# Optimization experiments

Hardware: AMD Instinct MI355X
Metric: run time of the kernel (lower is better)

The kernel has to match this reference:

```python
import jax, jax.numpy as jnp
import numpy as np
import math

SEQ = 2048
N_EMBD = 2048
N_HEAD = 16
DIM = N_EMBD // N_HEAD  # 128


def setup_inputs() -> dict:
    key = jax.random.key(0)
    k1, k2, k3, k4, k5 = jax.random.split(key, 5)
    s = 1.0 / math.sqrt(N_EMBD)
    return {
        "hidden_states": jax.random.normal(k1, (SEQ, N_EMBD), dtype=jnp.float32),
        "Wqkv": jax.random.normal(k2, (N_HEAD, N_EMBD, 3 * DIM), dtype=jnp.float32) * s,
        "bqkv": jax.random.normal(k3, (N_HEAD, 3 * DIM), dtype=jnp.float32) * 0.02,
        "Wout": jax.random.normal(k4, (N_EMBD, N_EMBD), dtype=jnp.float32) * s,
        "bout": jax.random.normal(k5, (N_EMBD,), dtype=jnp.float32) * 0.02,
    }


def reference(hidden_states, Wqkv, bqkv, Wout, bout):
    # per-head qkv projection: [h, s, 3*dim]
    qkv = jnp.einsum("se,hed->hsd", hidden_states, Wqkv) + bqkv[:, None, :]
    q, k, v = qkv[..., :DIM], qkv[..., DIM:2 * DIM], qkv[..., 2 * DIM:]
    # NOTE: original divides by sqrt(n_embd), not sqrt(head_dim)
    scale = 1.0 / math.sqrt(N_EMBD)
    scores = jnp.einsum("hsd,htd->hst", q, k) * scale  # [h, s, s]
    causal = jnp.tril(jnp.ones((SEQ, SEQ), dtype=bool))
    scores = jnp.where(causal[None], scores, -jnp.inf)
    probs = jax.nn.softmax(scores, axis=-1)
    out = jnp.einsum("hst,htd->hsd", probs, v)  # [h, s, dim]
    out = jnp.transpose(out, (1, 0, 2)).reshape(SEQ, N_EMBD)  # concat heads
    return out @ Wout + bout
```

## Files before the change

### kernel.cpp

```cpp
#include <hip/hip_runtime.h>
#include <cfloat>

#define SEQ   2048
#define NE    2048
#define NH    16
#define DIM   128
#define NKV   384
#define QSCALE 0.022097086912079611f

typedef __attribute__((ext_vector_type(8))) short bf16x8;
typedef __attribute__((ext_vector_type(4))) float f32x4;
typedef __attribute__((ext_vector_type(8))) unsigned short u16x8;

__device__ __forceinline__ unsigned short f32_to_bf16_rn(float x) {
    unsigned u = __builtin_bit_cast(unsigned, x);
    u += 0x7fffu + ((u >> 16) & 1u);
    return (unsigned short)(u >> 16);
}

__device__ __forceinline__ void gload16(const void* g, void* l) {
    __builtin_amdgcn_global_load_lds(
        (const __attribute__((address_space(1))) unsigned int*)g,
        (__attribute__((address_space(3))) unsigned int*)l, 16, 0, 0);
}

__global__ __launch_bounds__(256) void convert_bf16_kernel(
    const float* __restrict__ src, unsigned short* __restrict__ dst, int n4)
{
    for (int i = blockIdx.x * 256 + threadIdx.x; i < n4; i += gridDim.x * 256) {
        float4 x = ((const float4*)src)[i];
        ushort4 h;
        h.x = f32_to_bf16_rn(x.x);
        h.y = f32_to_bf16_rn(x.y);
        h.z = f32_to_bf16_rn(x.z);
        h.w = f32_to_bf16_rn(x.w);
        ((ushort4*)dst)[i] = h;
    }
}

__global__ __launch_bounds__(256) void transpose_bf16_kernel(
    const float* __restrict__ src, unsigned short* __restrict__ dst, int K, int N)
{
    const int kt = blockIdx.x, nt = blockIdx.y, b = blockIdx.z;
    const float* s = src + (size_t)b * K * N;
    __shared__ float tile[64][65];
    const int tid = threadIdx.x;
    #pragma unroll
    for (int i = 0; i < 4; i++) {
        int idx = tid + 256 * i;
        int kk = idx >> 4, n4 = idx & 15;
        float4 val = *(const float4*)&s[(size_t)(kt * 64 + kk) * N + nt * 64 + n4 * 4];
        tile[kk][n4 * 4 + 0] = val.x; tile[kk][n4 * 4 + 1] = val.y;
        tile[kk][n4 * 4 + 2] = val.z; tile[kk][n4 * 4 + 3] = val.w;
    }
    __syncthreads();
    #pragma unroll
    for (int i = 0; i < 2; i++) {
        int idx = tid + 256 * i;
        int nn = idx >> 3, k8 = idx & 7;
        u16x8 hv;
        #pragma unroll
        for (int j = 0; j < 8; j++)
            hv[j] = f32_to_bf16_rn(tile[k8 * 8 + j][nn]);
        size_t off = ((size_t)b * N + nt * 64 + nn) * K + kt * 64 + k8 * 8;
        *(u16x8*)&dst[off] = hv;
    }
}

template<int EPI>
__global__ __launch_bounds__(256, 2) void gemm_bf16_kernel(
    const unsigned short* __restrict__ A, const unsigned short* __restrict__ B,
    const float* __restrict__ bias, void* o0v, void* o1v, void* o2v)
{
    __shared__ unsigned short smem[2][128][64];
    const int tid = threadIdx.x;
    const int wave = tid >> 6, lane = tid & 63;
    const int s0 = blockIdx.x * 128, n0 = blockIdx.y * 128, z = blockIdx.z;
    const int bRowBase = (EPI == 0) ? (z * NKV + n0) : n0;

    const int srow = lane >> 3;
    const int sswz = ((lane & 7) ^ srow) << 4;
    size_t aoff[4], boff[4];
    #pragma unroll
    for (int j = 0; j < 4; j++) {
        int ra = s0 + wave * 32 + j * 8 + srow;
        int rb = bRowBase + wave * 32 + j * 8 + srow;
        aoff[j] = 2 * ((size_t)ra * NE) + sswz;
        boff[j] = 2 * ((size_t)rb * NE) + sswz;
    }
    const char* pA = (const char*)A;
    const char* pB = (const char*)B;

    f32x4 acc[4][4];
    #pragma unroll
    for (int i = 0; i < 4; i++)
        #pragma unroll
        for (int j = 0; j < 4; j++) acc[i][j] = (f32x4){0.f, 0.f, 0.f, 0.f};

    const int wm = wave >> 1, wn = wave & 1;
    const int fr = lane & 15, kg = lane >> 4;

    for (int k0 = 0; k0 < NE; k0 += 64) {
        #pragma unroll
        for (int j = 0; j < 4; j++) {
            gload16(pA + aoff[j], &smem[0][wave * 32 + j * 8][0]);
            gload16(pB + boff[j], &smem[1][wave * 32 + j * 8][0]);
            aoff[j] += 128; boff[j] += 128;
        }
        __syncthreads();

        #pragma unroll
        for (int kh = 0; kh < 2; kh++) {
            bf16x8 af[4], bf[4];
            #pragma unroll
            for (int f = 0; f < 4; f++) {
                int ra = wm * 64 + f * 16 + fr;
                int ca = ((kh * 4 + kg) ^ (ra & 7)) << 4;
                af[f] = *(const bf16x8*)((const char*)&smem[0][0][0] + ra * 128 + ca);
                int rb = wn * 64 + f * 16 + fr;
                int cb = ((kh * 4 + kg) ^ (rb & 7)) << 4;
                bf[f] = *(const bf16x8*)((const char*)&smem[1][0][0] + rb * 128 + cb);
            }
            #pragma unroll
            for (int fm = 0; fm < 4; fm++)
                #pragma unroll
                for (int fn = 0; fn < 4; fn++)
                    acc[fm][fn] = __builtin_amdgcn_mfma_f32_16x16x32_bf16(
                        af[fm], bf[fn], acc[fm][fn], 0, 0, 0);
        }
        __syncthreads();
    }

    #pragma unroll
    for (int fm = 0; fm < 4; fm++)
        #pragma unroll
        for (int fn = 0; fn < 4; fn++) {
            int col = wn * 64 + fn * 16 + fr;
            int row = wm * 64 + fm * 16 + kg * 4;
            if (EPI == 0) {
                const int seg = n0 >> 7;
                unsigned short* dst = (seg == 0) ? (unsigned short*)o0v
                                   : ((seg == 1) ? (unsigned short*)o1v
                                                 : (unsigned short*)o2v);
                const float mult = (seg == 0) ? QSCALE : 1.f;
                float bv = bias[z * NKV + n0 + col];
                #pragma unroll
                for (int r = 0; r < 4; r++)
                    dst[((size_t)(z * SEQ + s0 + row + r)) * DIM + col] =
                        f32_to_bf16_rn((acc[fm][fn][r] + bv) * mult);
            } else {
                float* out = (float*)o0v;
                float bv = bias[n0 + col];
                #pragma unroll
                for (int r = 0; r < 4; r++)
                    out[((size_t)(s0 + row + r)) * NE + n0 + col] = acc[fm][fn][r] + bv;
            }
        }
}

__global__ __launch_bounds__(256, 2) void attn_mfma_kernel(
    const unsigned short* __restrict__ Qb, const unsigned short* __restrict__ Kb,
    const unsigned short* __restrict__ Vb, unsigned short* __restrict__ AOb)
{
    const int lin = (int)blockIdx.x;
    const int halfg = lin >> 8;
    const int idx = lin & 255;
    const int qt = halfg ? (31 - (idx & 31)) : (idx & 31);
    const int h = (halfg << 3) + (idx >> 5);

    const char* kh = (const char*)(Kb + (size_t)h * SEQ * DIM);
    const unsigned short* vh = Vb + (size_t)h * SEQ * DIM;

    __shared__ __align__(16) unsigned short Klds[2][64 * 128];
    __shared__ __align__(16) unsigned short Vt[2][128][72];
    __shared__ __align__(16) unsigned short Plds[4][16][72];

    const int tid = threadIdx.x;
    const int w = tid >> 6, lane = tid & 63;
    const int fr = lane & 15, g = lane >> 4;
    const int qs = qt * 64;
    const int Q0 = qs + w * 16;

    bf16x8 qf[4];
    {
        const unsigned short* qrow = Qb + ((size_t)h * SEQ + Q0 + fr) * DIM;
        #pragma unroll
        for (int kc = 0; kc < 4; kc++)
            qf[kc] = *(const bf16x8*)&qrow[kc * 32 + g * 8];
    }

    const int key0 = (tid & 31) * 2;
    const int dbase = (tid >> 5) * 16;

    f32x4 oacc[8];
    #pragma unroll
    for (int d = 0; d < 8; d++) oacc[d] = (f32x4){0.f, 0.f, 0.f, 0.f};
    float m_run[4], l_run[4];
    #pragma unroll
    for (int r = 0; r < 4; r++) { m_run[r] = -FLT_MAX; l_run[r] = 0.f; }

    const int nt = qt + 1;
    u16x8 va0, va1, vc0, vc1;

    #pragma unroll
    for (int j = 0; j < 4; j++) {
        int row = w * 16 + j * 4 + g;
        gload16(kh + (size_t)row * 256 + ((fr ^ (row & 7)) << 4),
                &Klds[0][(w * 16 + j * 4) * 128]);
    }
    {
        const u16x8* r0 = (const u16x8*)&vh[(size_t)key0 * DIM + dbase];
        const u16x8* r1 = (const u16x8*)&vh[(size_t)(key0 + 1) * DIM + dbase];
        va0 = r0[0]; va1 = r0[1]; vc0 = r1[0]; vc1 = r1[1];
    }
    #pragma unroll
    for (int j = 0; j < 8; j++) {
        *(unsigned*)&Vt[0][dbase + j][key0]     = (unsigned)(unsigned short)va0[j] | ((unsigned)(unsigned short)vc0[j] << 16);
        *(unsigned*)&Vt[0][dbase + 8 + j][key0] = (unsigned)(unsigned short)va1[j] | ((unsigned)(unsigned short)vc1[j] << 16);
    }
    asm volatile("s_waitcnt vmcnt(0)" ::: "memory");

    for (int t = 0; t < nt; t++) {
        __syncthreads();
        const int buf = t & 1;
        const int t0 = t * 64;
        const bool last = (t == qt);

        if (!last) {
            const int t1 = t0 + 64;
            #pragma unroll
            for (int j = 0; j < 4; j++) {
                int row = w * 16 + j * 4 + g;
                gload16(kh + (size_t)(t1 + row) * 256 + ((fr ^ (row & 7)) << 4),
                        &Klds[buf ^ 1][(w * 16 + j * 4) * 128]);
            }
            const u16x8* r0 = (const u16x8*)&vh[(size_t)(t1 + key0) * DIM + dbase];
            const u16x8* r1 = (const u16x8*)&vh[(size_t)(t1 + key0 + 1) * DIM + dbase];
            va0 = r0[0]; va1 = r0[1]; vc0 = r1[0]; vc1 = r1[1];
        }

        f32x4 sacc[4];
        #pragma unroll
        for (int n4 = 0; n4 < 4; n4++) sacc[n4] = (f32x4){0.f, 0.f, 0.f, 0.f};
        #pragma unroll
        for (int n4 = 0; n4 < 4; n4++) {
            int rk = n4 * 16 + fr;
            #pragma unroll
            for (int kc = 0; kc < 4; kc++) {
                bf16x8 kf = *(const bf16x8*)((const char*)&Klds[buf][0] +
                                rk * 256 + (((kc * 4 + g) ^ (rk & 7)) << 4));
                sacc[n4] = __builtin_amdgcn_mfma_f32_16x16x32_bf16(
                    qf[kc], kf, sacc[n4], 0, 0, 0);
            }
        }

        if (last) {
            #pragma unroll
            for (int n4 = 0; n4 < 4; n4++) {
                int key = t0 + n4 * 16 + fr;
                #pragma unroll
                for (int r = 0; r < 4; r++) {
                    int q = Q0 + g * 4 + r;
                    sacc[n4][r] = (key > q) ? -3.0e38f : sacc[n4][r];
                }
            }
        }

        float mnew[4], sc[4];
        #pragma unroll
        for (int r = 0; r < 4; r++) {
            float mx = fmaxf(fmaxf(sacc[0][r], sacc[1][r]),
                             fmaxf(sacc[2][r], sacc[3][r]));
            mx = fmaxf(mx, __shfl_xor(mx, 1));
            mx = fmaxf(mx, __shfl_xor(mx, 2));
            mx = fmaxf(mx, __shfl_xor(mx, 4));
            mx = fmaxf(mx, __shfl_xor(mx, 8));
            mnew[r] = fmaxf(m_run[r], mx);
            sc[r] = __expf(m_run[r] - mnew[r]);
            m_run[r] = mnew[r];
        }
        float ps[4] = {0.f, 0.f, 0.f, 0.f};
        #pragma unroll
        for (int n4 = 0; n4 < 4; n4++)
            #pragma unroll
            for (int r = 0; r < 4; r++) {
                float p = __expf(sacc[n4][r] - mnew[r]);
                sacc[n4][r] = p;
                ps[r] += p;
            }
        #pragma unroll
        for (int r = 0; r < 4; r++) {
            float s = ps[r];
            s += __shfl_xor(s, 1);
            s += __shfl_xor(s, 2);
            s += __shfl_xor(s, 4);
            s += __shfl_xor(s, 8);
            l_run[r] = l_run[r] * sc[r] + s;
        }
        #pragma unroll
        for (int d = 0; d < 8; d++)
            #pragma unroll
            for (int r = 0; r < 4; r++) oacc[d][r] *= sc[r];

        #pragma unroll
        for (int n4 = 0; n4 < 4; n4++)
            #pragma unroll
            for (int r = 0; r < 4; r++)
                Plds[w][g * 4 + r][n4 * 16 + fr] = f32_to_bf16_rn(sacc[n4][r]);

        #pragma unroll
        for (int c = 0; c < 2; c++) {
            if (last && (t0 + c * 32 > Q0 + 15)) continue;
            bf16x8 pf = *(const bf16x8*)&Plds[w][fr][c * 32 + g * 8];
            #pragma unroll
            for (int dt = 0; dt < 8; dt++) {
                bf16x8 vf = *(const bf16x8*)&Vt[buf][dt * 16 + fr][c * 32 + g * 8];
                oacc[dt] = __builtin_amdgcn_mfma_f32_16x16x32_bf16(
                    pf, vf, oacc[dt], 0, 0, 0);
            }
        }

        if (!last) {
            #pragma unroll
            for (int j = 0; j < 8; j++) {
                *(unsigned*)&Vt[buf ^ 1][dbase + j][key0]     = (unsigned)(unsigned short)va0[j] | ((unsigned)(unsigned short)vc0[j] << 16);
                *(unsigned*)&Vt[buf ^ 1][dbase + 8 + j][key0] = (unsigned)(unsigned short)va1[j] | ((unsigned)(unsigned short)vc1[j] << 16);
            }
            asm volatile("s_waitcnt vmcnt(0)" ::: "memory");
        }
    }

    float inv[4];
    #pragma unroll
    for (int r = 0; r < 4; r++) inv[r] = 1.f / l_run[r];
    #pragma unroll
    for (int dt = 0; dt < 8; dt++)
        #pragma unroll
        for (int r = 0; r < 4; r++)
            AOb[(size_t)(Q0 + g * 4 + r) * NE + h * DIM + dt * 16 + fr] =
                f32_to_bf16_rn(oacc[dt][r] * inv[r]);
}

extern "C" void kernel_launch(void* const* d_in, const int* in_sizes, int n_in,
                              void* d_out, int out_size, void* d_ws, size_t ws_size,
                              hipStream_t stream) {
    const float* H    = (const float*)d_in[0];
    const float* Wqkv = (const float*)d_in[1];
    const float* bqkv = (const float*)d_in[2];
    const float* Wout = (const float*)d_in[3];
    const float* bout = (const float*)d_in[4];
    float* out = (float*)d_out;

    char* W8 = (char*)d_ws;
    const size_t MiB = 1ull << 20;
    unsigned short* qb  = (unsigned short*)(W8 + 0);
    unsigned short* kb  = (unsigned short*)(W8 + 8 * MiB);
    unsigned short* vb  = (unsigned short*)(W8 + 16 * MiB);
    unsigned short* Hb  = (unsigned short*)(W8 + 24 * MiB);
    unsigned short* AOb = (unsigned short*)(W8 + 32 * MiB);
    unsigned short* Wob = (unsigned short*)(W8 + 40 * MiB);
    unsigned short* Wqb = (unsigned short*)(W8 + 48 * MiB);

    convert_bf16_kernel<<<1024, 256, 0, stream>>>(H, Hb, SEQ * NE / 4);
    transpose_bf16_kernel<<<dim3(NE / 64, NKV / 64, NH), 256, 0, stream>>>(
        Wqkv, Wqb, NE, NKV);
    transpose_bf16_kernel<<<dim3(NE / 64, NE / 64, 1), 256, 0, stream>>>(
        Wout, Wob, NE, NE);
    gemm_bf16_kernel<0><<<dim3(SEQ / 128, NKV / 128, NH), 256, 0, stream>>>(
        Hb, Wqb, bqkv, qb, kb, vb);
    attn_mfma_kernel<<<dim3(512), 256, 0, stream>>>(qb, kb, vb, AOb);
    gemm_bf16_kernel<1><<<dim3(SEQ / 128, NE / 128, 1), 256, 0, stream>>>(
        AOb, Wob, bout, out, nullptr, nullptr);
}
```

Baseline: 188.4 us.

## Rewrite attention with 32x32 MFMA, two waves per block, register-resident P

Moves the attention kernel from 16x16x32 to 32x32x16 bf16 MFMA, computing S transposed so each lane owns a single query row. P stays in registers via v_cvt_pk_bf16 and permlane32_swap instead of an LDS round trip. Blocks shrink to 128 threads with 32 queries per wave, V is single-buffered behind two barriers, and MFMA sections get raised priority. The aim is fewer cross-lane shuffles, less LDS traffic and better MFMA throughput, at the cost of more registers per wave, fewer waves per block and serialised V staging.

```diff
diff --git a/kernel.cpp b/kernel.cpp
--- a/kernel.cpp
+++ b/kernel.cpp
@@ -10,12 +10,21 @@
 
 typedef __attribute__((ext_vector_type(8))) short bf16x8;
 typedef __attribute__((ext_vector_type(4))) float f32x4;
+typedef __attribute__((ext_vector_type(16))) float f32x16;
 typedef __attribute__((ext_vector_type(8))) unsigned short u16x8;
+typedef __attribute__((ext_vector_type(4))) unsigned int u32x4;
+typedef __attribute__((ext_vector_type(2))) unsigned int u32x2;
 
 __device__ __forceinline__ unsigned short f32_to_bf16_rn(float x) {
     unsigned u = __builtin_bit_cast(unsigned, x);
     u += 0x7fffu + ((u >> 16) & 1u);
     return (unsigned short)(u >> 16);
+}
+
+__device__ __forceinline__ unsigned cvt_pk_bf16(float lo, float hi) {
+    unsigned r;
+    asm("v_cvt_pk_bf16_f32 %0, %1, %2" : "=v"(r) : "v"(lo), "v"(hi));
+    return r;
 }
 
 __device__ __forceinline__ void gload16(const void* g, void* l) {
@@ -158,7 +167,7 @@
         }
 }
 
-__global__ __launch_bounds__(256, 2) void attn_mfma_kernel(
+__global__ __launch_bounds__(128, 2) void attn_mfma_kernel(
     const unsigned short* __restrict__ Qb, const unsigned short* __restrict__ Kb,
     const unsigned short* __restrict__ Vb, unsigned short* __restrict__ AOb)
 {
@@ -172,173 +181,175 @@
     const unsigned short* vh = Vb + (size_t)h * SEQ * DIM;
 
     __shared__ __align__(16) unsigned short Klds[2][64 * 128];
-    __shared__ __align__(16) unsigned short Vt[2][128][72];
-    __shared__ __align__(16) unsigned short Plds[4][16][72];
+    __shared__ __align__(16) unsigned short Vt[128][72];
 
     const int tid = threadIdx.x;
     const int w = tid >> 6, lane = tid & 63;
-    const int fr = lane & 15, g = lane >> 4;
+    const int c = lane & 31, hh = lane >> 5;
     const int qs = qt * 64;
-    const int Q0 = qs + w * 16;
-
-    bf16x8 qf[4];
+    const int Q0 = qs + w * 32;
+
+    bf16x8 qf[8];
     {
-        const unsigned short* qrow = Qb + ((size_t)h * SEQ + Q0 + fr) * DIM;
-        #pragma unroll
-        for (int kc = 0; kc < 4; kc++)
-            qf[kc] = *(const bf16x8*)&qrow[kc * 32 + g * 8];
+        const unsigned short* qrow = Qb + ((size_t)h * SEQ + Q0 + c) * DIM;
+        #pragma unroll
+        for (int st = 0; st < 8; st++)
+            qf[st] = *(const bf16x8*)&qrow[st * 16 + hh * 8];
     }
 
     const int key0 = (tid & 31) * 2;
-    const int dbase = (tid >> 5) * 16;
-
-    f32x4 oacc[8];
-    #pragma unroll
-    for (int d = 0; d < 8; d++) oacc[d] = (f32x4){0.f, 0.f, 0.f, 0.f};
-    float m_run[4], l_run[4];
-    #pragma unroll
-    for (int r = 0; r < 4; r++) { m_run[r] = -FLT_MAX; l_run[r] = 0.f; }
+    const int dbase = (tid >> 5) * 32;
+
+    f32x16 oacc[4];
+    #pragma unroll
+    for (int dt = 0; dt < 4; dt++)
+        #pragma unroll
+        for (int r = 0; r < 16; r++) oacc[dt][r] = 0.f;
+    float m_run = -FLT_MAX, l_run = 0.f;
 
     const int nt = qt + 1;
-    u16x8 va0, va1, vc0, vc1;
-
-    #pragma unroll
-    for (int j = 0; j < 4; j++) {
-        int row = w * 16 + j * 4 + g;
-        gload16(kh + (size_t)row * 256 + ((fr ^ (row & 7)) << 4),
-                &Klds[0][(w * 16 + j * 4) * 128]);
+    u16x8 vrA[4], vrB[4];
+
+    #pragma unroll
+    for (int j = 0; j < 8; j++) {
+        int row = w * 32 + j * 4 + (lane >> 4);
+        gload16(kh + (size_t)row * 256 + (((lane & 15) ^ (row & 7)) << 4),
+                &Klds[0][(w * 32 + j * 4) * 128]);
     }
     {
-        const u16x8* r0 = (const u16x8*)&vh[(size_t)key0 * DIM + dbase];
-        const u16x8* r1 = (const u16x8*)&vh[(size_t)(key0 + 1) * DIM + dbase];
-        va0 = r0[0]; va1 = r0[1]; vc0 = r1[0]; vc1 = r1[1];
-    }
-    #pragma unroll
-    for (int j = 0; j < 8; j++) {
-        *(unsigned*)&Vt[0][dbase + j][key0]     = (unsigned)(unsigned short)va0[j] | ((unsigned)(unsigned short)vc0[j] << 16);
-        *(unsigned*)&Vt[0][dbase + 8 + j][key0] = (unsigned)(unsigned short)va1[j] | ((unsigned)(unsigned short)vc1[j] << 16);
-    }
+        const u16x8* p0 = (const u16x8*)&vh[(size_t)key0 * DIM + dbase];
+        const u16x8* p1 = (const u16x8*)&vh[(size_t)(key0 + 1) * DIM + dbase];
+        #pragma unroll
+        for (int q8 = 0; q8 < 4; q8++) { vrA[q8] = p0[q8]; vrB[q8] = p1[q8]; }
+    }
+    #pragma unroll
+    for (int q8 = 0; q8 < 4; q8++)
+        #pragma unroll
+        for (int j = 0; j < 8; j++)
+            *(unsigned*)&Vt[dbase + q8 * 8 + j][key0] =
+                (unsigned)(unsigned short)vrA[q8][j] |
+                ((unsigned)(unsigned short)vrB[q8][j] << 16);
     asm volatile("s_waitcnt vmcnt(0)" ::: "memory");
+    __syncthreads();
 
     for (int t = 0; t < nt; t++) {
-        __syncthreads();
         const int buf = t & 1;
         const int t0 = t * 64;
-        const bool last = (t == qt);
-
-        if (!last) {
+        const bool notlast = (t + 1 < nt);
+
+        if (notlast) {
             const int t1 = t0 + 64;
             #pragma unroll
-            for (int j = 0; j < 4; j++) {
-                int row = w * 16 + j * 4 + g;
-                gload16(kh + (size_t)(t1 + row) * 256 + ((fr ^ (row & 7)) << 4),
-                        &Klds[buf ^ 1][(w * 16 + j * 4) * 128]);
-            }
-            const u16x8* r0 = (const u16x8*)&vh[(size_t)(t1 + key0) * DIM + dbase];
-            const u16x8* r1 = (const u16x8*)&vh[(size_t)(t1 + key0 + 1) * DIM + dbase];
-            va0 = r0[0]; va1 = r0[1]; vc0 = r1[0]; vc1 = r1[1];
-        }
-
-        f32x4 sacc[4];
-        #pragma unroll
-        for (int n4 = 0; n4 < 4; n4++) sacc[n4] = (f32x4){0.f, 0.f, 0.f, 0.f};
-        #pragma unroll
-        for (int n4 = 0; n4 < 4; n4++) {
-            int rk = n4 * 16 + fr;
-            #pragma unroll
-            for (int kc = 0; kc < 4; kc++) {
-                bf16x8 kf = *(const bf16x8*)((const char*)&Klds[buf][0] +
-                                rk * 256 + (((kc * 4 + g) ^ (rk & 7)) << 4));
-                sacc[n4] = __builtin_amdgcn_mfma_f32_16x16x32_bf16(
-                    qf[kc], kf, sacc[n4], 0, 0, 0);
-            }
-        }
-
-        if (last) {
-            #pragma unroll
-            for (int n4 = 0; n4 < 4; n4++) {
-                int key = t0 + n4 * 16 + fr;
+            for (int j = 0; j < 8; j++) {
+                int row = w * 32 + j * 4 + (lane >> 4);
+                gload16(kh + (size_t)(t1 + row) * 256 + (((lane & 15) ^ (row & 7)) << 4),
+                        &Klds[buf ^ 1][(w * 32 + j * 4) * 128]);
+            }
+            const u16x8* p0 = (const u16x8*)&vh[(size_t)(t1 + key0) * DIM + dbase];
+            const u16x8* p1 = (const u16x8*)&vh[(size_t)(t1 + key0 + 1) * DIM + dbase];
+            #pragma unroll
+            for (int q8 = 0; q8 < 4; q8++) { vrA[q8] = p0[q8]; vrB[q8] = p1[q8]; }
+        }
+
+        f32x16 s0, s1;
+        #pragma unroll
+        for (int r = 0; r < 16; r++) { s0[r] = 0.f; s1[r] = 0.f; }
+        __builtin_amdgcn_s_setprio(1);
+        #pragma unroll
+        for (int st = 0; st < 8; st++) {
+            int r0 = c, r1 = 32 + c;
+            bf16x8 kf0 = *(const bf16x8*)((const char*)&Klds[buf][0] +
+                            r0 * 256 + (((2 * st + hh) ^ (r0 & 7)) << 4));
+            bf16x8 kf1 = *(const bf16x8*)((const char*)&Klds[buf][0] +
+                            r1 * 256 + (((2 * st + hh) ^ (r1 & 7)) << 4));
+            s0 = __builtin_amdgcn_mfma_f32_32x32x16_bf16(kf0, qf[st], s0, 0, 0, 0);
+            s1 = __builtin_amdgcn_mfma_f32_32x32x16_bf16(kf1, qf[st], s1, 0, 0, 0);
+        }
+        __builtin_amdgcn_s_setprio(0);
+
+        if (!notlast) {
+            const int q = Q0 + c;
+            #pragma unroll
+            for (int r = 0; r < 16; r++) {
+                int krow = (r & 3) + 8 * (r >> 2) + 4 * hh;
+                s0[r] = (t0 + krow > q) ? -3.0e38f : s0[r];
+                s1[r] = (t0 + 32 + krow > q) ? -3.0e38f : s1[r];
+            }
+        }
+
+        float mx = s0[0];
+        #pragma unroll
+        for (int r = 1; r < 16; r++) mx = fmaxf(mx, s0[r]);
+        #pragma unroll
+        for (int r = 0; r < 16; r++) mx = fmaxf(mx, s1[r]);
+        mx = fmaxf(mx, __shfl_xor(mx, 32));
+        float m_new = fmaxf(m_run, mx);
+        float sc = __expf(m_run - m_new);
+        m_run = m_new;
+
+        float psum = 0.f;
+        #pragma unroll
+        for (int r = 0; r < 16; r++) {
+            s0[r] = __expf(s0[r] - m_new); psum += s0[r];
+        }
+        #pragma unroll
+        for (int r = 0; r < 16; r++) {
+            s1[r] = __expf(s1[r] - m_new); psum += s1[r];
+        }
+        psum += __shfl_xor(psum, 32);
+        l_run = l_run * sc + psum;
+        #pragma unroll
+        for (int dt = 0; dt < 4; dt++)
+            #pragma unroll
+            for (int r = 0; r < 16; r++) oacc[dt][r] *= sc;
+
+        unsigned pd[16];
+        #pragma unroll
+        for (int u = 0; u < 8; u++) {
+            pd[u]     = cvt_pk_bf16(s0[2 * u], s0[2 * u + 1]);
+            pd[8 + u] = cvt_pk_bf16(s1[2 * u], s1[2 * u + 1]);
+        }
+
+        __builtin_amdgcn_s_setprio(1);
+        #pragma unroll
+        for (int km = 0; km < 4; km++) {
+            u32x2 sA = __builtin_amdgcn_permlane32_swap(pd[4 * km + 0], pd[4 * km + 2], false, false);
+            u32x2 sB = __builtin_amdgcn_permlane32_swap(pd[4 * km + 1], pd[4 * km + 3], false, false);
+            u32x4 pw; pw[0] = sA[0]; pw[1] = sB[0]; pw[2] = sA[1]; pw[3] = sB[1];
+            bf16x8 pb = __builtin_bit_cast(bf16x8, pw);
+            #pragma unroll
+            for (int dt = 0; dt < 4; dt++) {
+                bf16x8 vf = *(const bf16x8*)&Vt[dt * 32 + c][km * 16 + hh * 8];
+                oacc[dt] = __builtin_amdgcn_mfma_f32_32x32x16_bf16(vf, pb, oacc[dt], 0, 0, 0);
+            }
+        }
+        __builtin_amdgcn_s_setprio(0);
+
+        if (notlast) {
+            __syncthreads();
+            #pragma unroll
+            for (int q8 = 0; q8 < 4; q8++)
                 #pragma unroll
-                for (int r = 0; r < 4; r++) {
-                    int q = Q0 + g * 4 + r;
-                    sacc[n4][r] = (key > q) ? -3.0e38f : sacc[n4][r];
-                }
-            }
-        }
-
-        float mnew[4], sc[4];
-        #pragma unroll
-        for (int r = 0; r < 4; r++) {
-            float mx = fmaxf(fmaxf(sacc[0][r], sacc[1][r]),
-                             fmaxf(sacc[2][r], sacc[3][r]));
-            mx = fmaxf(mx, __shfl_xor(mx, 1));
-            mx = fmaxf(mx, __shfl_xor(mx, 2));
-            mx = fmaxf(mx, __shfl_xor(mx, 4));
-            mx = fmaxf(mx, __shfl_xor(mx, 8));
-            mnew[r] = fmaxf(m_run[r], mx);
-            sc[r] = __expf(m_run[r] - mnew[r]);
-            m_run[r] = mnew[r];
-        }
-        float ps[4] = {0.f, 0.f, 0.f, 0.f};
-        #pragma unroll
-        for (int n4 = 0; n4 < 4; n4++)
-            #pragma unroll
-            for (int r = 0; r < 4; r++) {
-                float p = __expf(sacc[n4][r] - mnew[r]);
-                sacc[n4][r] = p;
-                ps[r] += p;
-            }
-        #pragma unroll
-        for (int r = 0; r < 4; r++) {
-            float s = ps[r];
-            s += __shfl_xor(s, 1);
-            s += __shfl_xor(s, 2);
-            s += __shfl_xor(s, 4);
-            s += __shfl_xor(s, 8);
-            l_run[r] = l_run[r] * sc[r] + s;
-        }
-        #pragma unroll
-        for (int d = 0; d < 8; d++)
-            #pragma unroll
-            for (int r = 0; r < 4; r++) oacc[d][r] *= sc[r];
-
-        #pragma unroll
-        for (int n4 = 0; n4 < 4; n4++)
-            #pragma unroll
-            for (int r = 0; r < 4; r++)
-                Plds[w][g * 4 + r][n4 * 16 + fr] = f32_to_bf16_rn(sacc[n4][r]);
-
-        #pragma unroll
-        for (int c = 0; c < 2; c++) {
-            if (last && (t0 + c * 32 > Q0 + 15)) continue;
-            bf16x8 pf = *(const bf16x8*)&Plds[w][fr][c * 32 + g * 8];
-            #pragma unroll
-            for (int dt = 0; dt < 8; dt++) {
-                bf16x8 vf = *(const bf16x8*)&Vt[buf][dt * 16 + fr][c * 32 + g * 8];
-                oacc[dt] = __builtin_amdgcn_mfma_f32_16x16x32_bf16(
-                    pf, vf, oacc[dt], 0, 0, 0);
-            }
-        }
-
-        if (!last) {
-            #pragma unroll
-            for (int j = 0; j < 8; j++) {
-                *(unsigned*)&Vt[buf ^ 1][dbase + j][key0]     = (unsigned)(unsigned short)va0[j] | ((unsigned)(unsigned short)vc0[j] << 16);
-                *(unsigned*)&Vt[buf ^ 1][dbase + 8 + j][key0] = (unsigned)(unsigned short)va1[j] | ((unsigned)(unsigned short)vc1[j] << 16);
-            }
+                for (int j = 0; j < 8; j++)
+                    *(unsigned*)&Vt[dbase + q8 * 8 + j][key0] =
+                        (unsigned)(unsigned short)vrA[q8][j] |
+                        ((unsigned)(unsigned short)vrB[q8][j] << 16);
             asm volatile("s_waitcnt vmcnt(0)" ::: "memory");
-        }
-    }
-
-    float inv[4];
-    #pragma unroll
-    for (int r = 0; r < 4; r++) inv[r] = 1.f / l_run[r];
-    #pragma unroll
-    for (int dt = 0; dt < 8; dt++)
-        #pragma unroll
-        for (int r = 0; r < 4; r++)
-            AOb[(size_t)(Q0 + g * 4 + r) * NE + h * DIM + dt * 16 + fr] =
-                f32_to_bf16_rn(oacc[dt][r] * inv[r]);
+            __syncthreads();
+        }
+    }
+
+    const float inv = 1.f / l_run;
+    unsigned short* aorow = AOb + (size_t)(Q0 + c) * NE + h * DIM;
+    #pragma unroll
+    for (int dt = 0; dt < 4; dt++)
+        #pragma unroll
+        for (int m = 0; m < 4; m++) {
+            unsigned lo = cvt_pk_bf16(oacc[dt][4 * m + 0] * inv, oacc[dt][4 * m + 1] * inv);
+            unsigned hi = cvt_pk_bf16(oacc[dt][4 * m + 2] * inv, oacc[dt][4 * m + 3] * inv);
+            u32x2 pk; pk[0] = lo; pk[1] = hi;
+            *(u32x2*)&aorow[dt * 32 + 8 * m + 4 * hh] = pk;
+        }
 }
 
 extern "C" void kernel_launch(void* const* d_in, const int* in_sizes, int n_in,
@@ -368,7 +379,7 @@
         Wout, Wob, NE, NE);
     gemm_bf16_kernel<0><<<dim3(SEQ / 128, NKV / 128, NH), 256, 0, stream>>>(
         Hb, Wqb, bqkv, qb, kb, vb);
-    attn_mfma_kernel<<<dim3(512), 256, 0, stream>>>(qb, kb, vb, AOb);
+    attn_mfma_kernel<<<dim3(512), 128, 0, stream>>>(qb, kb, vb, AOb);
     gemm_bf16_kernel<1><<<dim3(SEQ / 128, NE / 128, 1), 256, 0, stream>>>(
         AOb, Wob, bout, out, nullptr, nullptr);
 }
```

Measured after the change: 192.0 us. About the same (+1.9%).
